# Kernel optimization log

Measured on AMD Instinct MI355X. Metric: run time of the kernel, lower is better.

Reference implementation:

```python
import jax, jax.numpy as jnp
import numpy as np

N_NODES = 100000
N_EDGES = 1600000
IN_FEAT = 128
UNITS = 64


def setup_inputs() -> dict:
    key = jax.random.key(0)
    k1, k2, k3, k4, k5 = jax.random.split(key, 5)
    node_states = jax.random.normal(k1, (N_NODES, IN_FEAT), dtype=jnp.float32)
    # edges[:,0] is the destination/segment id; the original TF code's
    # repeat(bincount) normalization assumes edges sorted by edges[:,0].
    dst = jnp.sort(jax.random.randint(k2, (N_EDGES,), 0, N_NODES))
    src = jax.random.randint(k3, (N_EDGES,), 0, N_NODES)
    edges = jnp.stack([dst, src], axis=1).astype(jnp.int64)
    kernel = jax.random.normal(k4, (IN_FEAT, UNITS), dtype=jnp.float32) * 0.05
    kernel_attention = jax.random.normal(k5, (2 * UNITS, 1), dtype=jnp.float32) * 0.05
    return {"node_states": node_states, "edges": edges,
            "kernel": kernel, "kernel_attention": kernel_attention}


def reference(node_states, edges, kernel, kernel_attention):
    n_nodes = node_states.shape[0]
    dst = edges[:, 0]  # segment ids (aggregation target)
    src = edges[:, 1]  # neighbor being gathered

    h = node_states @ kernel                      # [N, U]
    h_dst = h[dst]                                # [E, U]
    h_src = h[src]                                # [E, U]
    # concat(h_dst, h_src) @ a  ==  h_dst @ a[:U] + h_src @ a[U:]
    u = kernel_attention.shape[0] // 2
    scores = (h_dst @ kernel_attention[:u] + h_src @ kernel_attention[u:])[:, 0]  # [E]
    scores = jax.nn.leaky_relu(scores, negative_slope=0.2)  # tf default alpha=0.2
    scores = jnp.exp(jnp.clip(scores, -2.0, 2.0))

    score_sum = jax.ops.segment_sum(scores, dst, num_segments=n_nodes)  # [N]
    attn = scores / score_sum[dst]                                      # [E]

    out = jax.ops.segment_sum(h_src * attn[:, None], dst, num_segments=n_nodes)  # [N, U]
    return out
```

## Files before the change

### kernel.cpp

```cpp
#include <hip/hip_runtime.h>
#include <hip/hip_bf16.h>

#define NN 100000
#define NE 1600000
#define NF 128
#define UU 64

typedef __attribute__((ext_vector_type(8))) short short8;
typedef __attribute__((ext_vector_type(4))) float f32x4;
typedef __attribute__((ext_vector_type(2))) float f32x2;
typedef __attribute__((ext_vector_type(4))) unsigned u32x4;

static const size_t OFF_H2   = 0;
static const size_t OFF_AD   = OFF_H2  + (size_t)NN * UU * 2;
static const size_t OFF_AS   = OFF_AD  + (size_t)NN * 4;
static const size_t OFF_ROW  = OFF_AS  + (size_t)NN * 4;

__device__ __forceinline__ unsigned cvtpk(float lo, float hi) {
    unsigned r;
    asm("v_cvt_pk_bf16_f32 %0, %1, %2" : "=v"(r) : "v"(lo), "v"(hi));
    return r;
}

__device__ __forceinline__ void pkfma(f32x2& acc, unsigned w32, float s) {
    f32x2 p, s2;
    p.x = __uint_as_float(w32 << 16);
    p.y = __uint_as_float(w32 & 0xFFFF0000u);
    s2.x = s; s2.y = s;
    acc = __builtin_elementwise_fma(p, s2, acc);
}

__device__ __forceinline__ int edge_flag(const int* ew) {
    int a = ew[2 * 400000 + 1] | ew[2 * 800000 + 1] |
            ew[2 * 1200000 + 1] | ew[2 * 1599999 + 1];
    return (a == 0) ? 1 : 0;
}

#define GEMM_BLOCKS   1563
#define ROWS_BLOCKS   391

__global__ __launch_bounds__(256) void mega(const float* __restrict__ X,
                                            const void* __restrict__ edges,
                                            const float* __restrict__ W,
                                            const float* __restrict__ ka,
                                            unsigned short* __restrict__ h2,
                                            float* __restrict__ a_dst,
                                            float* __restrict__ a_src,
                                            int* __restrict__ rows) {
    __shared__ unsigned Wl[4096];
    int bid = blockIdx.x;
    int tid = threadIdx.x;

    if (bid < GEMM_BLOCKS) {
        int wv = tid >> 6, lane = tid & 63;
        int quad = lane >> 4, l15 = lane & 15;
        int nb = bid * 64 + wv * 16;
        int row = nb + l15; if (row >= NN) row = NN - 1;
        const float* xr = X + (size_t)row * NF + quad * 8;

        float4 p0[4], p1[4];
#pragma unroll
        for (int kb = 0; kb < 4; kb++) {
            p0[kb] = *(const float4*)(xr + kb * 32);
            p1[kb] = *(const float4*)(xr + kb * 32 + 4);
        }

#pragma unroll
        for (int it = 0; it < 16; it++) {
            int d = it * 256 + tid;
            int i0 = d * 2;
            int j  = i0 & 7;
            int l  = (i0 >> 3) & 15;
            int q  = (i0 >> 7) & 3;
            int kb = (i0 >> 9) & 3;
            int nt = i0 >> 11;
            int r0 = kb * 32 + q * 8 + j;
            int c  = nt * 16 + l;
            float w0 = W[(size_t)r0 * UU + c];
            float w1 = W[(size_t)(r0 + 1) * UU + c];
            Wl[d] = cvtpk(w0, w1);
        }

        short8 afrag[4];
#pragma unroll
        for (int kb = 0; kb < 4; kb++) {
            u32x4 aw;
            aw[0] = cvtpk(p0[kb].x, p0[kb].y); aw[1] = cvtpk(p0[kb].z, p0[kb].w);
            aw[2] = cvtpk(p1[kb].x, p1[kb].y); aw[3] = cvtpk(p1[kb].z, p1[kb].w);
            afrag[kb] = __builtin_bit_cast(short8, aw);
        }
        __syncthreads();

        f32x4 acc[4] = {f32x4{0,0,0,0}, f32x4{0,0,0,0}, f32x4{0,0,0,0}, f32x4{0,0,0,0}};
        const short8* wl8 = (const short8*)Wl;
#pragma unroll
        for (int nt = 0; nt < 4; nt++) {
#pragma unroll
            for (int kb = 0; kb < 4; kb++) {
                short8 b = wl8[((nt * 4 + kb) * 4 + quad) * 16 + l15];
                acc[nt] = __builtin_amdgcn_mfma_f32_16x16x32_bf16(afrag[kb], b, acc[nt], 0, 0, 0);
            }
        }

        float kad[4], kas[4];
#pragma unroll
        for (int nt = 0; nt < 4; nt++) {
            kad[nt] = ka[nt * 16 + l15];
            kas[nt] = ka[64 + nt * 16 + l15];
        }
#pragma unroll
        for (int r = 0; r < 4; r++) {
            int m = nb + quad * 4 + r;
            if (m < NN) {
                uint2 v;
                v.x = cvtpk(acc[0][r], acc[1][r]);
                v.y = cvtpk(acc[2][r], acc[3][r]);
                *(uint2*)(h2 + (size_t)m * UU + l15 * 4) = v;
            }
            float pd = acc[0][r] * kad[0] + acc[1][r] * kad[1] + acc[2][r] * kad[2] + acc[3][r] * kad[3];
            float ps = acc[0][r] * kas[0] + acc[1][r] * kas[1] + acc[2][r] * kas[2] + acc[3][r] * kas[3];
            pd += __shfl_xor(pd, 1); pd += __shfl_xor(pd, 2);
            pd += __shfl_xor(pd, 4); pd += __shfl_xor(pd, 8);
            ps += __shfl_xor(ps, 1); ps += __shfl_xor(ps, 2);
            ps += __shfl_xor(ps, 4); ps += __shfl_xor(ps, 8);
            if (l15 == 0 && m < NN) { a_dst[m] = pd; a_src[m] = ps; }
        }
        return;
    }
    bid -= GEMM_BLOCKS;

    {
        int n = bid * 256 + tid;
        if (n > NN) return;
        const int* ew = (const int*)edges;
        if (n == NN) { rows[NN] = NE; return; }
        int fl = edge_flag(ew);
        int lo = 0, hi = NE;
        while (lo < hi) {
            int mid = (lo + hi) >> 1;
            int d = fl ? ew[4 * (size_t)mid] : ew[2 * (size_t)mid];
            if (d < n) lo = mid + 1; else hi = mid;
        }
        rows[n] = lo;
    }
}

__device__ __forceinline__ float edge_score(float ad, float as) {
    float sc = ad + as;
    sc = sc > 0.f ? sc : 0.2f * sc;
    sc = fminf(fmaxf(sc, -2.f), 2.f);
    return __expf(sc);
}

__global__ __launch_bounds__(256) void aggregate(const void* __restrict__ edges,
                                                 const int* __restrict__ rows,
                                                 const float* __restrict__ a_dst,
                                                 const float* __restrict__ a_src,
                                                 const unsigned short* __restrict__ h2,
                                                 float* __restrict__ out) {
    int tid = threadIdx.x;
    int lane = tid & 63;
    int g = lane >> 4, gl = lane & 15;
    int n = blockIdx.x * 16 + (tid >> 6) * 4 + g;
    if (n >= NN) return;
    int s = rows[n], e = rows[n + 1];
    int cnt = e - s;
    float ad = a_dst[n];
    const int* ew = (const int*)edges;
    int fl = edge_flag(ew);
    const int* sp = ew + (fl ? 2 : 1);
    int lsh = fl ? 2 : 1;
    const unsigned short* h2g = h2 + gl * 4;
    int gbase = g * 16;
    f32x2 acc01 = f32x2{0.f, 0.f};
    f32x2 acc23 = f32x2{0.f, 0.f};
    float inv;

#define BATCH(MS, MW, BOFF)                                                  \
    {                                                                        \
        uint2 rr[4]; float sw[4]; int sjv[4];                                \
        _Pragma("unroll")                                                    \
        for (int t = 0; t < 4; t++) {                                        \
            sjv[t] = __shfl(MS, gbase + (BOFF) + t);                         \
            sw[t]  = __shfl(MW, gbase + (BOFF) + t);                         \
        }                                                                    \
        _Pragma("unroll")                                                    \
        for (int t = 0; t < 4; t++)                                          \
            rr[t] = *(const uint2*)(h2g + (size_t)sjv[t] * UU);              \
        _Pragma("unroll")                                                    \
        for (int t = 0; t < 4; t++) {                                        \
            pkfma(acc01, rr[t].x, sw[t]);                                    \
            pkfma(acc23, rr[t].y, sw[t]);                                    \
        }                                                                    \
    }

    if (cnt <= 64) {
        int msrc[4];
#pragma unroll
        for (int k = 0; k < 4; k++) {
            int c = k * 16 + gl;
            msrc[k] = (c < cnt) ? sp[(size_t)(s + c) << lsh] : 0;
        }
        int sjv0[2][4];
#pragma unroll
        for (int b = 0; b < 2; b++)
#pragma unroll
            for (int t = 0; t < 4; t++)
                sjv0[b][t] = __shfl(msrc[0], gbase + b * 4 + t);
        uint2 rr0[2][4];
#pragma unroll
        for (int b = 0; b < 2; b++)
#pragma unroll
            for (int t = 0; t < 4; t++)
                rr0[b][t] = *(const uint2*)(h2g + (size_t)sjv0[b][t] * UU);
        float mw[4];
#pragma unroll
        for (int k = 0; k < 4; k++) {
            int c = k * 16 + gl;
            mw[k] = (c < cnt) ? edge_score(ad, a_src[msrc[k]]) : 0.f;
        }
#pragma unroll
        for (int b = 0; b < 2; b++) {
#pragma unroll
            for (int t = 0; t < 4; t++) {
                float w = __shfl(mw[0], gbase + b * 4 + t);
                pkfma(acc01, rr0[b][t].x, w);
                pkfma(acc23, rr0[b][t].y, w);
            }
        }
#pragma unroll
        for (int b = 2; b < 4; b++) {
            if (b * 4 < cnt) BATCH(msrc[0], mw[0], b * 4);
        }
#pragma unroll
        for (int k = 1; k < 4; k++) {
#pragma unroll
            for (int b = 0; b < 4; b++) {
                if (k * 16 + b * 4 < cnt) BATCH(msrc[k], mw[k], b * 4);
            }
        }
        float t0 = (mw[0] + mw[1]) + (mw[2] + mw[3]);
        t0 += __shfl_xor(t0, 1); t0 += __shfl_xor(t0, 2);
        t0 += __shfl_xor(t0, 4); t0 += __shfl_xor(t0, 8);
        inv = (cnt > 0) ? 1.f / t0 : 0.f;
    } else {
        float t0 = 0.f;
        for (int c = gl; c < cnt; c += 16) {
            int sj = sp[(size_t)(s + c) << lsh];
            t0 += edge_score(ad, a_src[sj]);
        }
        t0 += __shfl_xor(t0, 1); t0 += __shfl_xor(t0, 2);
        t0 += __shfl_xor(t0, 4); t0 += __shfl_xor(t0, 8);
        inv = 1.f / t0;
        for (int c0 = 0; c0 < cnt; c0 += 16) {
            int c = c0 + gl;
            int sj = 0; float w = 0.f;
            if (c < cnt) {
                sj = sp[(size_t)(s + c) << lsh];
                w = edge_score(ad, a_src[sj]);
            }
#pragma unroll
            for (int b = 0; b < 4; b++) {
                if (c0 + b * 4 < cnt) BATCH(sj, w, b * 4);
            }
        }
    }
#undef BATCH

    float* outr = out + (size_t)n * UU + gl;
    outr[0]  = acc01.x * inv;
    outr[16] = acc01.y * inv;
    outr[32] = acc23.x * inv;
    outr[48] = acc23.y * inv;
}

extern "C" void kernel_launch(void* const* d_in, const int* in_sizes, int n_in,
                              void* d_out, int out_size, void* d_ws, size_t ws_size,
                              hipStream_t stream) {
    const float* X  = (const float*)d_in[0];
    const void*  Ed = d_in[1];
    const float* W  = (const float*)d_in[2];
    const float* KA = (const float*)d_in[3];
    float* out = (float*)d_out;

    char* ws = (char*)d_ws;
    unsigned short* h2    = (unsigned short*)(ws + OFF_H2);
    float*          a_dst = (float*)(ws + OFF_AD);
    float*          a_src = (float*)(ws + OFF_AS);
    int*            rows  = (int*)(ws + OFF_ROW);

    mega<<<GEMM_BLOCKS + ROWS_BLOCKS, 256, 0, stream>>>(
        X, Ed, W, KA, h2, a_dst, a_src, rows);
    aggregate<<<(NN + 15) / 16, 256, 0, stream>>>(Ed, rows, a_dst, a_src, h2, out);
}
```

Measured before the change: 143.0 us.

## Widen aggregate gathers to 16-byte loads across two edges per step

The aggregation kernel now gives each 16-lane group two edges per step, with each half-group loading 16 bytes (uint4) per lane from the bf16 neighbor row instead of 8 bytes. This halves the number of gather steps per edge batch and reduces instruction and shuffle overhead per edge. The two halves' partial sums are combined with a cross-lane xor-shuffle and written as float2 stores. The weight-staging loop in the GEMM part also switches to float4 loads of W, which cuts its load count by four.

```diff
diff --git a/kernel.cpp b/kernel.cpp
--- a/kernel.cpp
+++ b/kernel.cpp
@@ -66,19 +66,22 @@
         }
 
 #pragma unroll
-        for (int it = 0; it < 16; it++) {
-            int d = it * 256 + tid;
-            int i0 = d * 2;
-            int j  = i0 & 7;
-            int l  = (i0 >> 3) & 15;
-            int q  = (i0 >> 7) & 3;
-            int kb = (i0 >> 9) & 3;
-            int nt = i0 >> 11;
-            int r0 = kb * 32 + q * 8 + j;
-            int c  = nt * 16 + l;
-            float w0 = W[(size_t)r0 * UU + c];
-            float w1 = W[(size_t)(r0 + 1) * UU + c];
-            Wl[d] = cvtpk(w0, w1);
+        for (int it = 0; it < 4; it++) {
+            int qi = it * 256 + tid;
+            int j2 = qi & 3;
+            int l4 = (qi >> 2) & 3;
+            int q  = (qi >> 4) & 3;
+            int kb = (qi >> 6) & 3;
+            int nt = (qi >> 8) & 3;
+            int r0 = kb * 32 + q * 8 + 2 * j2;
+            int c0 = nt * 16 + l4 * 4;
+            float4 w0 = *(const float4*)(W + (size_t)r0 * UU + c0);
+            float4 w1 = *(const float4*)(W + (size_t)(r0 + 1) * UU + c0);
+            int dbase = (nt << 10) | (kb << 8) | (q << 6) | (l4 << 4) | j2;
+            Wl[dbase]      = cvtpk(w0.x, w1.x);
+            Wl[dbase + 4]  = cvtpk(w0.y, w1.y);
+            Wl[dbase + 8]  = cvtpk(w0.z, w1.z);
+            Wl[dbase + 12] = cvtpk(w0.w, w1.w);
         }
 
         short8 afrag[4];
@@ -161,6 +164,7 @@
     int tid = threadIdx.x;
     int lane = tid & 63;
     int g = lane >> 4, gl = lane & 15;
+    int a = gl & 7, hi = gl >> 3;
     int n = blockIdx.x * 16 + (tid >> 6) * 4 + g;
     if (n >= NN) return;
     int s = rows[n], e = rows[n + 1];
@@ -170,28 +174,19 @@
     int fl = edge_flag(ew);
     const int* sp = ew + (fl ? 2 : 1);
     int lsh = fl ? 2 : 1;
-    const unsigned short* h2g = h2 + gl * 4;
     int gbase = g * 16;
-    f32x2 acc01 = f32x2{0.f, 0.f};
-    f32x2 acc23 = f32x2{0.f, 0.f};
+    int esel0 = gbase + hi;
+    f32x2 accA = f32x2{0.f, 0.f}, accB = f32x2{0.f, 0.f};
+    f32x2 accC = f32x2{0.f, 0.f}, accD = f32x2{0.f, 0.f};
     float inv;
 
-#define BATCH(MS, MW, BOFF)                                                  \
+#define PSTEP(MS, MW, ST)                                                    \
     {                                                                        \
-        uint2 rr[4]; float sw[4]; int sjv[4];                                \
-        _Pragma("unroll")                                                    \
-        for (int t = 0; t < 4; t++) {                                        \
-            sjv[t] = __shfl(MS, gbase + (BOFF) + t);                         \
-            sw[t]  = __shfl(MW, gbase + (BOFF) + t);                         \
-        }                                                                    \
-        _Pragma("unroll")                                                    \
-        for (int t = 0; t < 4; t++)                                          \
-            rr[t] = *(const uint2*)(h2g + (size_t)sjv[t] * UU);              \
-        _Pragma("unroll")                                                    \
-        for (int t = 0; t < 4; t++) {                                        \
-            pkfma(acc01, rr[t].x, sw[t]);                                    \
-            pkfma(acc23, rr[t].y, sw[t]);                                    \
-        }                                                                    \
+        int sjv = __shfl(MS, esel0 + (ST) * 2);                              \
+        float wv = __shfl(MW, esel0 + (ST) * 2);                             \
+        uint4 rr = *((const uint4*)(h2 + (size_t)sjv * UU) + a);             \
+        pkfma(accA, rr.x, wv); pkfma(accB, rr.y, wv);                        \
+        pkfma(accC, rr.z, wv); pkfma(accD, rr.w, wv);                        \
     }
 
     if (cnt <= 64) {
@@ -201,18 +196,14 @@
             int c = k * 16 + gl;
             msrc[k] = (c < cnt) ? sp[(size_t)(s + c) << lsh] : 0;
         }
-        int sjv0[2][4];
-#pragma unroll
-        for (int b = 0; b < 2; b++)
-#pragma unroll
-            for (int t = 0; t < 4; t++)
-                sjv0[b][t] = __shfl(msrc[0], gbase + b * 4 + t);
-        uint2 rr0[2][4];
-#pragma unroll
-        for (int b = 0; b < 2; b++)
-#pragma unroll
-            for (int t = 0; t < 4; t++)
-                rr0[b][t] = *(const uint2*)(h2g + (size_t)sjv0[b][t] * UU);
+        int sj0[4];
+#pragma unroll
+        for (int st = 0; st < 4; st++)
+            sj0[st] = __shfl(msrc[0], esel0 + st * 2);
+        uint4 pf[4];
+#pragma unroll
+        for (int st = 0; st < 4; st++)
+            pf[st] = *((const uint4*)(h2 + (size_t)sj0[st] * UU) + a);
         float mw[4];
 #pragma unroll
         for (int k = 0; k < 4; k++) {
@@ -220,23 +211,20 @@
             mw[k] = (c < cnt) ? edge_score(ad, a_src[msrc[k]]) : 0.f;
         }
 #pragma unroll
-        for (int b = 0; b < 2; b++) {
-#pragma unroll
-            for (int t = 0; t < 4; t++) {
-                float w = __shfl(mw[0], gbase + b * 4 + t);
-                pkfma(acc01, rr0[b][t].x, w);
-                pkfma(acc23, rr0[b][t].y, w);
-            }
-        }
-#pragma unroll
-        for (int b = 2; b < 4; b++) {
-            if (b * 4 < cnt) BATCH(msrc[0], mw[0], b * 4);
+        for (int st = 0; st < 4; st++) {
+            float wv = __shfl(mw[0], esel0 + st * 2);
+            pkfma(accA, pf[st].x, wv); pkfma(accB, pf[st].y, wv);
+            pkfma(accC, pf[st].z, wv); pkfma(accD, pf[st].w, wv);
+        }
+#pragma unroll
+        for (int st = 4; st < 8; st++) {
+            if (st * 2 < cnt) PSTEP(msrc[0], mw[0], st);
         }
 #pragma unroll
         for (int k = 1; k < 4; k++) {
 #pragma unroll
-            for (int b = 0; b < 4; b++) {
-                if (k * 16 + b * 4 < cnt) BATCH(msrc[k], mw[k], b * 4);
+            for (int st = 0; st < 8; st++) {
+                if (k * 16 + st * 2 < cnt) PSTEP(msrc[k], mw[k], st);
             }
         }
         float t0 = (mw[0] + mw[1]) + (mw[2] + mw[3]);
@@ -260,18 +248,26 @@
                 w = edge_score(ad, a_src[sj]);
             }
 #pragma unroll
-            for (int b = 0; b < 4; b++) {
-                if (c0 + b * 4 < cnt) BATCH(sj, w, b * 4);
-            }
-        }
-    }
-#undef BATCH
-
-    float* outr = out + (size_t)n * UU + gl;
-    outr[0]  = acc01.x * inv;
-    outr[16] = acc01.y * inv;
-    outr[32] = acc23.x * inv;
-    outr[48] = acc23.y * inv;
+            for (int st = 0; st < 8; st++) {
+                if (c0 + st * 2 < cnt) PSTEP(sj, w, st);
+            }
+        }
+    }
+#undef PSTEP
+
+    accA.x += __shfl_xor(accA.x, 8); accA.y += __shfl_xor(accA.y, 8);
+    accB.x += __shfl_xor(accB.x, 8); accB.y += __shfl_xor(accB.y, 8);
+    accC.x += __shfl_xor(accC.x, 8); accC.y += __shfl_xor(accC.y, 8);
+    accD.x += __shfl_xor(accD.x, 8); accD.y += __shfl_xor(accD.y, 8);
+
+    float* outr = out + (size_t)n * UU;
+    if (hi == 0) {
+        *(float2*)(outr + 2 * a)      = make_float2(accA.x * inv, accC.x * inv);
+        *(float2*)(outr + 16 + 2 * a) = make_float2(accA.y * inv, accC.y * inv);
+    } else {
+        *(float2*)(outr + 32 + 2 * a) = make_float2(accB.x * inv, accD.x * inv);
+        *(float2*)(outr + 48 + 2 * a) = make_float2(accB.y * inv, accD.y * inv);
+    }
 }
 
 extern "C" void kernel_launch(void* const* d_in, const int* in_sizes, int n_in,
```

Result: slower. 146.8 us (+2.7%).
